# Performance work log

Hardware: AMD Instinct MI355X
Metric: run time of the kernel (lower is better)

## Reference

```python
import jax, jax.numpy as jnp
import numpy as np

N_NODES = 50000
N_EDGES = 800000
N_REL = 16
N_GRAPHS = 64
IN_DIM = 128
HID = 128
FC = 256
N_CLASSES = 16


def setup_inputs() -> dict:
    key = jax.random.key(0)
    ks = jax.random.split(key, 16)
    h = jax.random.normal(ks[0], (N_NODES, IN_DIM), dtype=jnp.float32)
    src = jax.random.randint(ks[1], (N_EDGES,), 0, N_NODES, dtype=jnp.int32)
    dst = jax.random.randint(ks[2], (N_EDGES,), 0, N_NODES, dtype=jnp.int32)
    rel_types = jax.random.randint(ks[3], (N_EDGES,), 0, N_REL, dtype=jnp.int32)
    graph_ids = jnp.sort(jax.random.randint(ks[4], (N_NODES,), 0, N_GRAPHS, dtype=jnp.int32))
    s1 = 1.0 / np.sqrt(IN_DIM)
    s2 = 1.0 / np.sqrt(HID)
    # RGCN layer 1: per-relation weights, self-loop weight, bias
    W1 = jax.random.normal(ks[5], (N_REL, IN_DIM, HID), dtype=jnp.float32) * s1
    Ws1 = jax.random.normal(ks[6], (IN_DIM, HID), dtype=jnp.float32) * s1
    b1 = jnp.zeros((HID,), dtype=jnp.float32)
    # RGCN layer 2
    W2 = jax.random.normal(ks[7], (N_REL, HID, HID), dtype=jnp.float32) * s2
    Ws2 = jax.random.normal(ks[8], (HID, HID), dtype=jnp.float32) * s2
    b2 = jnp.zeros((HID,), dtype=jnp.float32)
    # FC layer after mean pooling
    Wfc = jax.random.normal(ks[9], (HID, FC), dtype=jnp.float32) * s2
    bfc = jnp.zeros((FC,), dtype=jnp.float32)
    # classify head
    Wc = jax.random.normal(ks[10], (FC, N_CLASSES), dtype=jnp.float32) * (1.0 / np.sqrt(FC))
    bc = jnp.zeros((N_CLASSES,), dtype=jnp.float32)
    return dict(h=h, src=src, dst=dst, rel_types=rel_types, graph_ids=graph_ids,
                W1=W1, Ws1=Ws1, b1=b1, W2=W2, Ws2=Ws2, b2=b2,
                Wfc=Wfc, bfc=bfc, Wc=Wc, bc=bc)


def _rel_graph_conv(h, W, Ws, b, src, dst, rel):
    # dgl RelGraphConv (regularizer=None, self_loop=True, bias=True):
    # out[v] = sum_{e:(u->v)} W[rel_e] @ h[u] + Ws @ h[v] + b
    hW = jnp.einsum('ni,rio->rno', h, W)            # [R, N, out]
    msg = hW[rel, src]                               # [E, out] gather per edge
    agg = jax.ops.segment_sum(msg, dst, num_segments=N_NODES)
    return agg + h @ Ws + b


def _mean_nodes(h, graph_ids):
    sums = jax.ops.segment_sum(h, graph_ids, num_segments=N_GRAPHS)      # [G, D]
    cnts = jax.ops.segment_sum(jnp.ones((h.shape[0], 1), h.dtype), graph_ids,
                               num_segments=N_GRAPHS)                    # [G, 1]
    return sums / jnp.maximum(cnts, 1.0)


def reference(h, src, dst, rel_types, graph_ids,
              W1, Ws1, b1, W2, Ws2, b2, Wfc, bfc, Wc, bc):
    h = h.astype(jnp.float32)
    h = jax.nn.relu(_rel_graph_conv(h, W1, Ws1, b1, src, dst, rel_types))
    h = jax.nn.relu(_rel_graph_conv(h, W2, Ws2, b2, src, dst, rel_types))
    hg = _mean_nodes(h, graph_ids)                   # [G, HID]
    hg = jax.nn.relu(hg @ Wfc + bfc)                 # [G, FC]
    return jax.nn.softmax(hg @ Wc + bc, axis=1)      # [G, n_classes]
```

## Files before the change

kernel.cpp:

```cpp
#include <hip/hip_runtime.h>
#include <hip/hip_bf16.h>

#define N_NODES   50000
#define N_PAD     50048
#define N_EDGES   800000
#define N_REL     16
#define N_GRAPHS  64
#define DIM       128
#define FC_DIM    256
#define N_CLASSES 16

#define SB        50176
#define NBINS_P   (16 * SB)
#define NBLK_PP   784
#define NBINS_D   50176
#define NBLK_PD   49
#define POOL_CH   64
#define MAXBLK_A  13294

#define WS_MARK   0
#define WS_HISTD  802816
#define WS_HG     1003520
#define WS_CNT    1036288
#define WS_SRCOF  1036544
#define MEMSET_SZ 4239616
#define WS_OFFSD  4239616
#define WS_CURD   4440576
#define WS_PARTD  4641280
#define WS_PARTP  4641536
#define WS_BLKB   4644864
#define WS_RELB   4648192
#define WS_CIDMAP 4648448
#define WS_RECS   7859712
#define WS_X1     11059712
#define WS_X2     23872000
#define WS_AGG    36684288
#define WS_WB     49496576
#define WS_T      50610688

#define XW_TOTAL  (N_PAD * DIM + 2 * 17 * 16384)

typedef __attribute__((ext_vector_type(8))) short bf16x8;
typedef __attribute__((ext_vector_type(4))) float f32x4;

__device__ __forceinline__ void atomAddF(float* p, float v) {
#if defined(__gfx90a__) || defined(__gfx942__) || defined(__gfx950__)
    unsafeAtomicAdd(p, v);
#else
    atomicAdd(p, v);
#endif
}

__device__ __forceinline__ float bf2f(unsigned int u) {
    union { float f; unsigned int i; } x; x.i = u << 16; return x.f;
}
__device__ __forceinline__ unsigned short f2bf(float f) {
    union { float f; unsigned int u; } x; x.f = f;
    unsigned int r = x.u + 0x7fff + ((x.u >> 16) & 1);
    return (unsigned short)(r >> 16);
}
__device__ __forceinline__ void accum8(float* qa, uint4 u) {
    qa[0] += bf2f(u.x & 0xffff); qa[1] += bf2f(u.x >> 16);
    qa[2] += bf2f(u.y & 0xffff); qa[3] += bf2f(u.y >> 16);
    qa[4] += bf2f(u.z & 0xffff); qa[5] += bf2f(u.z >> 16);
    qa[6] += bf2f(u.w & 0xffff); qa[7] += bf2f(u.w >> 16);
}
__device__ __forceinline__ void pack16(const float* qa, unsigned short* dst) {
    #pragma unroll
    for (int j = 0; j < 2; ++j) {
        uint4 w;
        w.x = ((unsigned int)f2bf(qa[j*8+1]) << 16) | f2bf(qa[j*8+0]);
        w.y = ((unsigned int)f2bf(qa[j*8+3]) << 16) | f2bf(qa[j*8+2]);
        w.z = ((unsigned int)f2bf(qa[j*8+5]) << 16) | f2bf(qa[j*8+4]);
        w.w = ((unsigned int)f2bf(qa[j*8+7]) << 16) | f2bf(qa[j*8+6]);
        ((uint4*)dst)[j] = w;
    }
}

__global__ void k_convXW(const float* __restrict__ h, unsigned short* __restrict__ x1,
                         const float* __restrict__ W1, const float* __restrict__ Ws1,
                         const float* __restrict__ W2, const float* __restrict__ Ws2,
                         unsigned short* __restrict__ Wb) {
    int id = blockIdx.x * blockDim.x + threadIdx.x;
    if (id < N_PAD * DIM) {
        int v = id >> 7;
        x1[id] = (v < N_NODES) ? f2bf(h[id]) : (unsigned short)0;
    } else {
        int t = id - N_PAD * DIM;
        int l = t / 278528, rem = t % 278528;
        int r = rem >> 14, rr = rem & 16383;
        int n = rr >> 7, k = rr & 127;
        const float* W  = l ? W2 : W1;
        const float* Ws = l ? Ws2 : Ws1;
        float v = (r < 16) ? W[r * 16384 + k * 128 + n] : Ws[k * 128 + n];
        Wb[t] = f2bf(v);
    }
}

__global__ void k_hist2(const int* __restrict__ src, const int* __restrict__ dst,
                        const int* __restrict__ rel,
                        unsigned char* __restrict__ mark, int* __restrict__ histD) {
    int e = blockIdx.x * blockDim.x + threadIdx.x;
    if (e < N_EDGES) {
        atomicAdd(&histD[dst[e]], 1);
        mark[rel[e] * SB + src[e]] = 1;
    }
}

__global__ void k_scanA(const int* __restrict__ hist, int* __restrict__ partials) {
    __shared__ int red[256];
    int b = blockIdx.x, t = threadIdx.x;
    int4 v = ((const int4*)(hist + b * 1024))[t];
    red[t] = v.x + v.y + v.z + v.w;
    __syncthreads();
    for (int o = 128; o > 0; o >>= 1) {
        if (t < o) red[t] += red[t + o];
        __syncthreads();
    }
    if (t == 0) partials[b] = red[0];
}

__global__ void k_scanB(int* __restrict__ partials, int* __restrict__ offs_tail) {
    __shared__ int s1[256], s2[256];
    int t = threadIdx.x;
    int v = (t < NBLK_PD) ? partials[t] : 0;
    s1[t] = v; __syncthreads();
    int* cur = s1; int* nxt = s2;
    for (int o = 1; o < 256; o <<= 1) {
        nxt[t] = cur[t] + ((t >= o) ? cur[t - o] : 0);
        __syncthreads();
        int* tmp = cur; cur = nxt; nxt = tmp;
    }
    if (t < NBLK_PD) partials[t] = cur[t] - v;
    if (t == 255) offs_tail[0] = cur[255];
}

__global__ void k_scanC(const int* __restrict__ hist, const int* __restrict__ partials,
                        int* __restrict__ offs, int* __restrict__ curp) {
    __shared__ int s1[256], s2[256];
    int b = blockIdx.x, t = threadIdx.x;
    int4 v = ((const int4*)(hist + b * 1024))[t];
    int sum = v.x + v.y + v.z + v.w;
    s1[t] = sum; __syncthreads();
    int* cur = s1; int* nxt = s2;
    for (int o = 1; o < 256; o <<= 1) {
        nxt[t] = cur[t] + ((t >= o) ? cur[t - o] : 0);
        __syncthreads();
        int* tmp = cur; cur = nxt; nxt = tmp;
    }
    int base = partials[b] + cur[t] - sum;
    int4 w;
    w.x = base;
    w.y = base + v.x;
    w.z = w.y + v.y;
    w.w = w.z + v.z;
    ((int4*)(offs + b * 1024))[t] = w;
    ((int4*)(curp + b * 1024))[t] = w;
}

__global__ void k_scanPA(const unsigned int* __restrict__ markU, int* __restrict__ partP) {
    __shared__ int red[256];
    int b = blockIdx.x, t = threadIdx.x;
    unsigned int u = markU[b * 256 + t];
    red[t] = (int)((u & 1) + ((u >> 8) & 1) + ((u >> 16) & 1) + ((u >> 24) & 1));
    __syncthreads();
    for (int o = 128; o > 0; o >>= 1) {
        if (t < o) red[t] += red[t + o];
        __syncthreads();
    }
    if (t == 0) partP[b] = red[0];
}

__global__ void k_scanPB(const int* __restrict__ partP, int* __restrict__ blkB,
                         int* __restrict__ relB) {
    __shared__ int s1[784], s2[784];
    __shared__ int tot[16], rbase[17];
    int t = threadIdx.x;
    int rel = t / 49, pos = t - rel * 49;
    int v = (t < 784) ? partP[t] : 0;
    if (t < 784) s1[t] = v;
    __syncthreads();
    int* cur = s1; int* nxt = s2;
    for (int o = 1; o < 64; o <<= 1) {
        if (t < 784) nxt[t] = cur[t] + ((pos >= o) ? cur[t - o] : 0);
        __syncthreads();
        int* tmp = cur; cur = nxt; nxt = tmp;
    }
    if (t < 784 && pos == 48) tot[rel] = cur[t];
    __syncthreads();
    if (t == 0) {
        int base = 0;
        for (int r = 0; r < 16; ++r) { rbase[r] = base; base += (tot[r] + 63) & ~63; }
        rbase[16] = base;
    }
    __syncthreads();
    if (t < 784) blkB[t] = rbase[rel] + cur[t] - v;
    if (t < 17)  relB[t] = rbase[t];
}

__global__ void k_scanPC(const unsigned int* __restrict__ markU, const int* __restrict__ blkB,
                         int* __restrict__ cidMap, int* __restrict__ srcOf) {
    __shared__ int s1[256], s2[256];
    int b = blockIdx.x, t = threadIdx.x;
    unsigned int u = markU[b * 256 + t];
    int f0 = (int)(u & 1), f1 = (int)((u >> 8) & 1);
    int f2 = (int)((u >> 16) & 1), f3 = (int)((u >> 24) & 1);
    int sum = f0 + f1 + f2 + f3;
    s1[t] = sum; __syncthreads();
    int* cur = s1; int* nxt = s2;
    for (int o = 1; o < 256; o <<= 1) {
        nxt[t] = cur[t] + ((t >= o) ? cur[t - o] : 0);
        __syncthreads();
        int* tmp = cur; cur = nxt; nxt = tmp;
    }
    int cid = blkB[b] + cur[t] - sum;
    int rel = b / 49;
    int key0 = b * 1024 + t * 4;
    int srcBase = key0 - rel * SB;
    if (f0) { cidMap[key0]     = cid; srcOf[cid] = srcBase;     cid++; }
    if (f1) { cidMap[key0 + 1] = cid; srcOf[cid] = srcBase + 1; cid++; }
    if (f2) { cidMap[key0 + 2] = cid; srcOf[cid] = srcBase + 2; cid++; }
    if (f3) { cidMap[key0 + 3] = cid; srcOf[cid] = srcBase + 3; cid++; }
}

__global__ void k_scatterK(const int* __restrict__ src, const int* __restrict__ dst,
                           const int* __restrict__ rel, const int* __restrict__ cidMap,
                           int* __restrict__ curD, unsigned int* __restrict__ recs) {
    int e = blockIdx.x * blockDim.x + threadIdx.x;
    if (e < N_EDGES) {
        int cid = cidMap[rel[e] * SB + src[e]];
        int pos = atomicAdd(&curD[dst[e]], 1);
        recs[pos] = (unsigned int)cid;
    }
}

__global__ __launch_bounds__(256) void k_phaseA(
    const unsigned short* __restrict__ x, const unsigned short* __restrict__ Wb,
    const int* __restrict__ srcOf, const int* __restrict__ relB,
    unsigned short* __restrict__ T)
{
    __shared__ unsigned short Xs[64 * 136];
    __shared__ unsigned short Cs[64 * 136];
    __shared__ int sSrc[64];
    __shared__ int sRB[17];

    int tid = threadIdx.x;
    if (tid < 17) sRB[tid] = relB[tid];
    __syncthreads();

    int row0 = blockIdx.x * 64;
    int rtot = sRB[16];
    if (row0 >= rtot + N_PAD) return;

    int r = 16;
    #pragma unroll
    for (int i = 0; i < 16; ++i)
        if (row0 < sRB[i + 1]) { r = i; break; }

    if (tid < 64) sSrc[tid] = (r == 16) ? (row0 - rtot + tid) : srcOf[row0 + tid];
    __syncthreads();

    {
        int row = tid >> 2, c0 = tid & 3;
        const uint4* xp = (const uint4*)(x + (size_t)sSrc[row] * DIM);
        uint4* lp = (uint4*)(&Xs[row * 136]);
        #pragma unroll
        for (int i = 0; i < 4; ++i) lp[c0 + 4 * i] = xp[c0 + 4 * i];
    }
    __syncthreads();

    int w = tid >> 6, l = tid & 63;
    int nl = l & 15, q = l >> 4;

    bf16x8 Bf[2][4];
    const unsigned short* wr = Wb + r * 16384;
    #pragma unroll
    for (int nt = 0; nt < 2; ++nt) {
        int n = w * 32 + nt * 16 + nl;
        #pragma unroll
        for (int kc = 0; kc < 4; ++kc)
            Bf[nt][kc] = *(const bf16x8*)(wr + n * 128 + kc * 32 + q * 8);
    }
    #pragma unroll
    for (int m = 0; m < 4; ++m) {
        f32x4 a0 = {0.f,0.f,0.f,0.f}, a1 = {0.f,0.f,0.f,0.f};
        #pragma unroll
        for (int kc = 0; kc < 4; ++kc) {
            bf16x8 a = *(const bf16x8*)(&Xs[(m * 16 + nl) * 136 + kc * 32 + q * 8]);
            a0 = __builtin_amdgcn_mfma_f32_16x16x32_bf16(a, Bf[0][kc], a0, 0, 0, 0);
            a1 = __builtin_amdgcn_mfma_f32_16x16x32_bf16(a, Bf[1][kc], a1, 0, 0, 0);
        }
        int col = w * 32 + nl;
        #pragma unroll
        for (int reg = 0; reg < 4; ++reg) {
            int row = m * 16 + q * 4 + reg;
            Cs[row * 136 + col]      = f2bf(a0[reg]);
            Cs[row * 136 + col + 16] = f2bf(a1[reg]);
        }
    }
    __syncthreads();
    {
        unsigned short* Tb = T + (size_t)row0 * DIM;
        #pragma unroll
        for (int it = 0; it < 4; ++it) {
            int c = tid + it * 256;
            int row = c >> 4, k8 = c & 15;
            uint4 vv = *(const uint4*)(&Cs[row * 136 + k8 * 8]);
            *(uint4*)(Tb + row * DIM + k8 * 8) = vv;
        }
    }
}

__global__ __launch_bounds__(256) void k_phaseB(
    const unsigned short* __restrict__ T, const unsigned int* __restrict__ recs,
    const int* __restrict__ offsD, const int* __restrict__ relB,
    const float* __restrict__ bias,
    unsigned short* __restrict__ aggOut, int relu)
{
    __shared__ int sOffs[33];
    __shared__ float sBias[128];
    __shared__ int sSelf;
    int tid = threadIdx.x;
    int v0 = blockIdx.x * 32;
    if (tid < 33) sOffs[tid] = offsD[v0 + tid];
    if (tid == 40) sSelf = relB[16];
    if (tid >= 64 && tid < 96) ((float4*)sBias)[tid - 64] = ((const float4*)bias)[tid - 64];
    __syncthreads();

    int g = tid >> 3, s = tid & 7;
    int dst = v0 + g;
    float qa[16];
    #pragma unroll
    for (int i = 0; i < 16; ++i) qa[i] = sBias[s * 16 + i];

    int beg = sOffs[g], end = sOffs[g + 1];
    int e = beg;
    for (; e + 3 < end; e += 4) {
        unsigned int c0 = recs[e], c1 = recs[e+1], c2 = recs[e+2], c3 = recs[e+3];
        const uint4* t0 = (const uint4*)(T + (size_t)c0 * DIM + s * 16);
        const uint4* t1 = (const uint4*)(T + (size_t)c1 * DIM + s * 16);
        const uint4* t2 = (const uint4*)(T + (size_t)c2 * DIM + s * 16);
        const uint4* t3 = (const uint4*)(T + (size_t)c3 * DIM + s * 16);
        uint4 a0 = t0[0], a1 = t0[1], b0 = t1[0], b1 = t1[1];
        uint4 cc0 = t2[0], cc1 = t2[1], d0 = t3[0], d1 = t3[1];
        accum8(qa, a0); accum8(qa + 8, a1);
        accum8(qa, b0); accum8(qa + 8, b1);
        accum8(qa, cc0); accum8(qa + 8, cc1);
        accum8(qa, d0); accum8(qa + 8, d1);
    }
    for (; e < end; ++e) {
        unsigned int c = recs[e];
        const uint4* tp = (const uint4*)(T + (size_t)c * DIM + s * 16);
        uint4 u0 = tp[0], u1 = tp[1];
        accum8(qa, u0); accum8(qa + 8, u1);
    }
    {
        const uint4* tp = (const uint4*)(T + (size_t)(sSelf + dst) * DIM + s * 16);
        uint4 u0 = tp[0], u1 = tp[1];
        accum8(qa, u0); accum8(qa + 8, u1);
    }

    if (relu) {
        #pragma unroll
        for (int i = 0; i < 16; ++i) qa[i] = fmaxf(qa[i], 0.f);
    }
    pack16(qa, aggOut + (size_t)dst * DIM + s * 16);
}

__global__ void k_pool(const unsigned short* __restrict__ agg2, const int* __restrict__ gids,
                       float* __restrict__ hg_sum, int* __restrict__ cnt)
{
    int d  = threadIdx.x;
    int n0 = blockIdx.x * POOL_CH;
    int nend = min(n0 + POOL_CH, N_NODES);
    if (n0 >= N_NODES) return;
    int curg = gids[n0];
    float run = 0.f;
    for (int n = n0; n < nend; ++n) {
        int g = gids[n];
        if (g != curg) { atomAddF(&hg_sum[curg*DIM + d], run); run = 0.f; curg = g; }
        run += fmaxf(bf2f((unsigned int)agg2[n*DIM + d]), 0.f);
    }
    atomAddF(&hg_sum[curg*DIM + d], run);
    if (d == 0) {
        int cg = gids[n0]; int rl = 0;
        for (int n = n0; n < nend; ++n) {
            int g = gids[n];
            if (g != cg) { atomicAdd(&cnt[cg], rl); rl = 0; cg = g; }
            rl++;
        }
        atomicAdd(&cnt[cg], rl);
    }
}

__global__ __launch_bounds__(256) void k_head(
    const float* __restrict__ hg_sum, const int* __restrict__ cnt,
    const float* __restrict__ Wfc, const float* __restrict__ bfc,
    const float* __restrict__ Wc, const float* __restrict__ bc,
    float* __restrict__ out)
{
    int g = blockIdx.x, t = threadIdx.x;
    __shared__ float hgl[DIM];
    __shared__ float fcl[FC_DIM];
    __shared__ float lg[N_CLASSES];
    if (t < DIM) {
        float c = (float)max(cnt[g], 1);
        hgl[t] = hg_sum[g*DIM + t] / c;
    }
    __syncthreads();
    {
        float sv = bfc[t];
        #pragma unroll 4
        for (int k = 0; k < DIM; ++k) sv += hgl[k] * Wfc[k*FC_DIM + t];
        fcl[t] = fmaxf(sv, 0.f);
    }
    __syncthreads();
    if (t < N_CLASSES) {
        float lgt = bc[t];
        #pragma unroll 4
        for (int k = 0; k < FC_DIM; ++k) lgt += fcl[k] * Wc[k*N_CLASSES + t];
        lg[t] = lgt;
    }
    __syncthreads();
    if (t < N_CLASSES) {
        float m = lg[0];
        #pragma unroll
        for (int c = 1; c < N_CLASSES; ++c) m = fmaxf(m, lg[c]);
        float sden = 0.f;
        #pragma unroll
        for (int c = 0; c < N_CLASSES; ++c) sden += expf(lg[c] - m);
        out[g*N_CLASSES + t] = expf(lg[t] - m) / sden;
    }
}

extern "C" void kernel_launch(void* const* d_in, const int* in_sizes, int n_in,
                              void* d_out, int out_size, void* d_ws, size_t ws_size,
                              hipStream_t stream)
{
    const float* h   = (const float*)d_in[0];
    const int*   src = (const int*)d_in[1];
    const int*   dst = (const int*)d_in[2];
    const int*   rel = (const int*)d_in[3];
    const int*   gid = (const int*)d_in[4];
    const float* W1  = (const float*)d_in[5];
    const float* Ws1 = (const float*)d_in[6];
    const float* b1  = (const float*)d_in[7];
    const float* W2  = (const float*)d_in[8];
    const float* Ws2 = (const float*)d_in[9];
    const float* b2  = (const float*)d_in[10];
    const float* Wfc = (const float*)d_in[11];
    const float* bfc = (const float*)d_in[12];
    const float* Wc  = (const float*)d_in[13];
    const float* bc  = (const float*)d_in[14];
    float* out = (float*)d_out;

    char* ws = (char*)d_ws;
    unsigned char* mark = (unsigned char*)(ws + WS_MARK);
    int*   histD = (int*)(ws + WS_HISTD);
    float* hgsum = (float*)(ws + WS_HG);
    int*   cnt   = (int*)(ws + WS_CNT);
    int*   srcOf = (int*)(ws + WS_SRCOF);
    int*   offsD = (int*)(ws + WS_OFFSD);
    int*   curD  = (int*)(ws + WS_CURD);
    int*   partD = (int*)(ws + WS_PARTD);
    int*   partP = (int*)(ws + WS_PARTP);
    int*   blkB  = (int*)(ws + WS_BLKB);
    int*   relB  = (int*)(ws + WS_RELB);
    int*   cidMap= (int*)(ws + WS_CIDMAP);
    unsigned int* recs = (unsigned int*)(ws + WS_RECS);
    unsigned short* x1  = (unsigned short*)(ws + WS_X1);
    unsigned short* x2  = (unsigned short*)(ws + WS_X2);
    unsigned short* agg = (unsigned short*)(ws + WS_AGG);
    unsigned short* Wb  = (unsigned short*)(ws + WS_WB);
    unsigned short* T   = (unsigned short*)(ws + WS_T);

    int gridA = MAXBLK_A;
    if (ws_size > (size_t)WS_T) {
        long long capRows = (long long)((ws_size - WS_T) / 256);
        long long capBlk = capRows / 64;
        if (capBlk < gridA) gridA = (int)capBlk;
    }

    hipMemsetAsync(mark, 0, MEMSET_SZ, stream);

    k_convXW<<<XW_TOTAL / 256, 256, 0, stream>>>(h, x1, W1, Ws1, W2, Ws2, Wb);
    k_hist2<<<(N_EDGES + 255) / 256, 256, 0, stream>>>(src, dst, rel, mark, histD);

    k_scanA<<<NBLK_PD, 256, 0, stream>>>(histD, partD);
    k_scanB<<<1, 256, 0, stream>>>(partD, offsD + NBINS_D);
    k_scanC<<<NBLK_PD, 256, 0, stream>>>(histD, partD, offsD, curD);

    k_scanPA<<<NBLK_PP, 256, 0, stream>>>((const unsigned int*)mark, partP);
    k_scanPB<<<1, 1024, 0, stream>>>(partP, blkB, relB);
    k_scanPC<<<NBLK_PP, 256, 0, stream>>>((const unsigned int*)mark, blkB, cidMap, srcOf);

    k_scatterK<<<(N_EDGES + 255) / 256, 256, 0, stream>>>(src, dst, rel, cidMap, curD, recs);

    k_phaseA<<<gridA, 256, 0, stream>>>(x1, Wb, srcOf, relB, T);
    k_phaseB<<<N_PAD / 32, 256, 0, stream>>>(T, recs, offsD, relB, b1, x2, 1);
    k_phaseA<<<gridA, 256, 0, stream>>>(x2, Wb + 17 * 16384, srcOf, relB, T);
    k_phaseB<<<N_PAD / 32, 256, 0, stream>>>(T, recs, offsD, relB, b2, agg, 0);

    k_pool<<<(N_PAD + POOL_CH - 1) / POOL_CH, 128, 0, stream>>>(agg, gid, hgsum, cnt);
    k_head<<<N_GRAPHS, 256, 0, stream>>>(hgsum, cnt, Wfc, bfc, Wc, bc, out);
}
```

Measured before the change: 455.0 us.

## Replace global-atomic CSR build with two-pass coarse/fine bucket sort by destination

Replaces the per-edge global atomic histogram on destination plus the three-kernel scan and atomic scatter with a two-level counting sort. Coarse buckets of 64 destinations are counted per edge chunk in shared memory, scanned in one block, and edges are scattered into coarse segments. A second pass then sorts within each segment using shared-memory atomics and writes the fine offsets. The goal is to cut contended global atomics and kernel launches. The cost is an extra temporary record pass, only 98 blocks in the chunked kernels, and a serial per-column loop in the single-block scan.

```diff
diff --git a/kernel.cpp b/kernel.cpp
--- a/kernel.cpp
+++ b/kernel.cpp
@@ -13,30 +13,31 @@
 #define SB        50176
 #define NBINS_P   (16 * SB)
 #define NBLK_PP   784
-#define NBINS_D   50176
-#define NBLK_PD   49
+#define NCOARSE   782
+#define NCH       98
+#define CHSZ      8192
 #define POOL_CH   64
 #define MAXBLK_A  13294
 
 #define WS_MARK   0
-#define WS_HISTD  802816
-#define WS_HG     1003520
-#define WS_CNT    1036288
-#define WS_SRCOF  1036544
-#define MEMSET_SZ 4239616
-#define WS_OFFSD  4239616
-#define WS_CURD   4440576
-#define WS_PARTD  4641280
-#define WS_PARTP  4641536
-#define WS_BLKB   4644864
-#define WS_RELB   4648192
-#define WS_CIDMAP 4648448
-#define WS_RECS   7859712
-#define WS_X1     11059712
-#define WS_X2     23872000
-#define WS_AGG    36684288
-#define WS_WB     49496576
-#define WS_T      50610688
+#define WS_HG     802816
+#define WS_CNT    835584
+#define WS_SRCOF  835840
+#define MEMSET_SZ 4038912
+#define WS_BLKH   4038912
+#define WS_COFS   4345600
+#define WS_PARTP  4348928
+#define WS_BLKB   4352256
+#define WS_RELB   4355584
+#define WS_CIDMAP 4355840
+#define WS_RTMP   7567104
+#define WS_RECS   10767104
+#define WS_OFFSD  13967104
+#define WS_X1     14167552
+#define WS_X2     26979840
+#define WS_AGG    39792128
+#define WS_WB     52604416
+#define WS_T      53718528
 
 #define XW_TOTAL  (N_PAD * DIM + 2 * 17 * 16384)
 
@@ -97,65 +98,51 @@
     }
 }
 
-__global__ void k_hist2(const int* __restrict__ src, const int* __restrict__ dst,
-                        const int* __restrict__ rel,
-                        unsigned char* __restrict__ mark, int* __restrict__ histD) {
-    int e = blockIdx.x * blockDim.x + threadIdx.x;
-    if (e < N_EDGES) {
-        atomicAdd(&histD[dst[e]], 1);
+__global__ __launch_bounds__(256) void k_h1(
+    const int* __restrict__ src, const int* __restrict__ dst, const int* __restrict__ rel,
+    unsigned char* __restrict__ mark, int* __restrict__ blockHist)
+{
+    __shared__ int hl[NCOARSE];
+    int b = blockIdx.x, t = threadIdx.x;
+    for (int i = t; i < NCOARSE; i += 256) hl[i] = 0;
+    __syncthreads();
+    int e0 = b * CHSZ;
+    int eend = min(e0 + CHSZ, N_EDGES);
+    for (int e = e0 + t; e < eend; e += 256) {
+        int d = dst[e];
         mark[rel[e] * SB + src[e]] = 1;
-    }
-}
-
-__global__ void k_scanA(const int* __restrict__ hist, int* __restrict__ partials) {
-    __shared__ int red[256];
-    int b = blockIdx.x, t = threadIdx.x;
-    int4 v = ((const int4*)(hist + b * 1024))[t];
-    red[t] = v.x + v.y + v.z + v.w;
-    __syncthreads();
-    for (int o = 128; o > 0; o >>= 1) {
-        if (t < o) red[t] += red[t + o];
-        __syncthreads();
-    }
-    if (t == 0) partials[b] = red[0];
-}
-
-__global__ void k_scanB(int* __restrict__ partials, int* __restrict__ offs_tail) {
-    __shared__ int s1[256], s2[256];
+        atomicAdd(&hl[d >> 6], 1);
+    }
+    __syncthreads();
+    for (int i = t; i < NCOARSE; i += 256) blockHist[b * NCOARSE + i] = hl[i];
+}
+
+__global__ void k_cscan(int* __restrict__ blockHist, int* __restrict__ coarseOffs) {
+    __shared__ int s1[1024], s2[1024];
     int t = threadIdx.x;
-    int v = (t < NBLK_PD) ? partials[t] : 0;
-    s1[t] = v; __syncthreads();
+    int tot = 0;
+    if (t < NCOARSE) {
+        int run = 0;
+        for (int b = 0; b < NCH; ++b) {
+            int v = blockHist[b * NCOARSE + t];
+            blockHist[b * NCOARSE + t] = run;
+            run += v;
+        }
+        tot = run;
+    }
+    s1[t] = tot; __syncthreads();
     int* cur = s1; int* nxt = s2;
-    for (int o = 1; o < 256; o <<= 1) {
+    for (int o = 1; o < 1024; o <<= 1) {
         nxt[t] = cur[t] + ((t >= o) ? cur[t - o] : 0);
         __syncthreads();
         int* tmp = cur; cur = nxt; nxt = tmp;
     }
-    if (t < NBLK_PD) partials[t] = cur[t] - v;
-    if (t == 255) offs_tail[0] = cur[255];
-}
-
-__global__ void k_scanC(const int* __restrict__ hist, const int* __restrict__ partials,
-                        int* __restrict__ offs, int* __restrict__ curp) {
-    __shared__ int s1[256], s2[256];
-    int b = blockIdx.x, t = threadIdx.x;
-    int4 v = ((const int4*)(hist + b * 1024))[t];
-    int sum = v.x + v.y + v.z + v.w;
-    s1[t] = sum; __syncthreads();
-    int* cur = s1; int* nxt = s2;
-    for (int o = 1; o < 256; o <<= 1) {
-        nxt[t] = cur[t] + ((t >= o) ? cur[t - o] : 0);
-        __syncthreads();
-        int* tmp = cur; cur = nxt; nxt = tmp;
-    }
-    int base = partials[b] + cur[t] - sum;
-    int4 w;
-    w.x = base;
-    w.y = base + v.x;
-    w.z = w.y + v.y;
-    w.w = w.z + v.z;
-    ((int4*)(offs + b * 1024))[t] = w;
-    ((int4*)(curp + b * 1024))[t] = w;
+    if (t < NCOARSE) {
+        int base = cur[t] - tot;
+        coarseOffs[t] = base;
+        for (int b = 0; b < NCH; ++b) blockHist[b * NCOARSE + t] += base;
+    }
+    if (t == NCOARSE) coarseOffs[NCOARSE] = cur[NCOARSE - 1];
 }
 
 __global__ void k_scanPA(const unsigned int* __restrict__ markU, int* __restrict__ partP) {
@@ -223,14 +210,53 @@
     if (f3) { cidMap[key0 + 3] = cid; srcOf[cid] = srcBase + 3; cid++; }
 }
 
-__global__ void k_scatterK(const int* __restrict__ src, const int* __restrict__ dst,
-                           const int* __restrict__ rel, const int* __restrict__ cidMap,
-                           int* __restrict__ curD, unsigned int* __restrict__ recs) {
-    int e = blockIdx.x * blockDim.x + threadIdx.x;
-    if (e < N_EDGES) {
+__global__ __launch_bounds__(256) void k_scat1(
+    const int* __restrict__ src, const int* __restrict__ dst, const int* __restrict__ rel,
+    const int* __restrict__ cidMap, const int* __restrict__ blockHist,
+    unsigned int* __restrict__ rtmp)
+{
+    __shared__ int baseL[NCOARSE];
+    __shared__ int hl[NCOARSE];
+    int b = blockIdx.x, t = threadIdx.x;
+    for (int i = t; i < NCOARSE; i += 256) { baseL[i] = blockHist[b * NCOARSE + i]; hl[i] = 0; }
+    __syncthreads();
+    int e0 = b * CHSZ;
+    int eend = min(e0 + CHSZ, N_EDGES);
+    for (int e = e0 + t; e < eend; e += 256) {
+        int d = dst[e];
         int cid = cidMap[rel[e] * SB + src[e]];
-        int pos = atomicAdd(&curD[dst[e]], 1);
-        recs[pos] = (unsigned int)cid;
+        int c = d >> 6;
+        int rank = atomicAdd(&hl[c], 1);
+        rtmp[baseL[c] + rank] = ((unsigned int)cid << 6) | (unsigned int)(d & 63);
+    }
+}
+
+__global__ __launch_bounds__(256) void k_p2(
+    const unsigned int* __restrict__ rtmp, const int* __restrict__ coarseOffs,
+    unsigned int* __restrict__ recs, int* __restrict__ offsD)
+{
+    __shared__ int cntL[64], exclL[65], cur2[64];
+    int i = blockIdx.x, t = threadIdx.x;
+    int segB = coarseOffs[i], segE = coarseOffs[i + 1];
+    if (t < 64) { cntL[t] = 0; cur2[t] = 0; }
+    __syncthreads();
+    for (int e = segB + t; e < segE; e += 256)
+        atomicAdd(&cntL[rtmp[e] & 63u], 1);
+    __syncthreads();
+    if (t == 0) {
+        int run = segB;
+        #pragma unroll
+        for (int d = 0; d < 64; ++d) { exclL[d] = run; run += cntL[d]; }
+        exclL[64] = run;
+    }
+    __syncthreads();
+    if (t < 64) offsD[i * 64 + t] = exclL[t];
+    if (t == 64) offsD[i * 64 + 64] = exclL[64];
+    for (int e = segB + t; e < segE; e += 256) {
+        unsigned int r = rtmp[e];
+        int d = (int)(r & 63u);
+        int rank = atomicAdd(&cur2[d], 1);
+        recs[exclL[d] + rank] = r >> 6;
     }
 }
 
@@ -456,18 +482,18 @@
 
     char* ws = (char*)d_ws;
     unsigned char* mark = (unsigned char*)(ws + WS_MARK);
-    int*   histD = (int*)(ws + WS_HISTD);
     float* hgsum = (float*)(ws + WS_HG);
     int*   cnt   = (int*)(ws + WS_CNT);
     int*   srcOf = (int*)(ws + WS_SRCOF);
-    int*   offsD = (int*)(ws + WS_OFFSD);
-    int*   curD  = (int*)(ws + WS_CURD);
-    int*   partD = (int*)(ws + WS_PARTD);
+    int*   blkH  = (int*)(ws + WS_BLKH);
+    int*   cOffs = (int*)(ws + WS_COFS);
     int*   partP = (int*)(ws + WS_PARTP);
     int*   blkB  = (int*)(ws + WS_BLKB);
     int*   relB  = (int*)(ws + WS_RELB);
     int*   cidMap= (int*)(ws + WS_CIDMAP);
+    unsigned int* rtmp = (unsigned int*)(ws + WS_RTMP);
     unsigned int* recs = (unsigned int*)(ws + WS_RECS);
+    int*   offsD = (int*)(ws + WS_OFFSD);
     unsigned short* x1  = (unsigned short*)(ws + WS_X1);
     unsigned short* x2  = (unsigned short*)(ws + WS_X2);
     unsigned short* agg = (unsigned short*)(ws + WS_AGG);
@@ -484,17 +510,15 @@
     hipMemsetAsync(mark, 0, MEMSET_SZ, stream);
 
     k_convXW<<<XW_TOTAL / 256, 256, 0, stream>>>(h, x1, W1, Ws1, W2, Ws2, Wb);
-    k_hist2<<<(N_EDGES + 255) / 256, 256, 0, stream>>>(src, dst, rel, mark, histD);
-
-    k_scanA<<<NBLK_PD, 256, 0, stream>>>(histD, partD);
-    k_scanB<<<1, 256, 0, stream>>>(partD, offsD + NBINS_D);
-    k_scanC<<<NBLK_PD, 256, 0, stream>>>(histD, partD, offsD, curD);
-
+    k_h1<<<NCH, 256, 0, stream>>>(src, dst, rel, mark, blkH);
+
+    k_cscan<<<1, 1024, 0, stream>>>(blkH, cOffs);
     k_scanPA<<<NBLK_PP, 256, 0, stream>>>((const unsigned int*)mark, partP);
     k_scanPB<<<1, 1024, 0, stream>>>(partP, blkB, relB);
     k_scanPC<<<NBLK_PP, 256, 0, stream>>>((const unsigned int*)mark, blkB, cidMap, srcOf);
 
-    k_scatterK<<<(N_EDGES + 255) / 256, 256, 0, stream>>>(src, dst, rel, cidMap, curD, recs);
+    k_scat1<<<NCH, 256, 0, stream>>>(src, dst, rel, cidMap, blkH, rtmp);
+    k_p2<<<NCOARSE, 256, 0, stream>>>(rtmp, cOffs, recs, offsD);
 
     k_phaseA<<<gridA, 256, 0, stream>>>(x1, Wb, srcOf, relB, T);
     k_phaseB<<<N_PAD / 32, 256, 0, stream>>>(T, recs, offsD, relB, b1, x2, 1);
```

Result: faster. 437.0 us (-3.9%).
